# Performance work log

Measured on AMD Instinct MI355X. Metric: run time of the kernel, lower is better.

The kernel has to match this reference:

```python
import jax, jax.numpy as jnp
import numpy as np


def setup_inputs() -> dict:
    key = jax.random.key(0)
    k1, k2, k3, k4 = jax.random.split(key, 4)
    B, C, H, W = 32, 1, 512, 512
    return {
        "cancer_logits": jax.random.normal(k1, (B, C, H, W), dtype=jnp.float32),
        "label": jax.random.uniform(k2, (B,), dtype=jnp.float32),
        "prostate_mask": jax.random.uniform(k3, (B, 1, H, W), dtype=jnp.float32),
        "needle_mask": jax.random.uniform(k4, (B, 1, H, W), dtype=jnp.float32),
    }


def reference(cancer_logits, label, prostate_mask, needle_mask):
    # Valid region = prostate AND needle masks thresholded at 0.5.
    mask = (prostate_mask > 0.5) & (needle_mask > 0.5)          # [B,1,H,W] bool
    x = cancer_logits                                            # [B,1,H,W]
    y = label[:, None, None, None]                               # broadcast per-core label to pixels
    # Numerically-stable BCE with logits: max(x,0) - x*y + log(1+exp(-|x|))
    bce = jnp.maximum(x, 0.0) - x * y + jnp.log1p(jnp.exp(-jnp.abs(x)))
    m = mask.astype(x.dtype)
    # Mean over the selected (valid) elements == sum(bce*m)/count, same as
    # F.binary_cross_entropy_with_logits on the gathered logits/labels.
    count = jnp.maximum(jnp.sum(m), 1.0)
    return jnp.sum(bce * m) / count
```

## Files before the change

kernel.cpp:

```cpp
#include <hip/hip_runtime.h>
#include <math.h>

constexpr int HW_SIZE = 512 * 512;
constexpr int NB      = 32;
constexpr int N       = NB * HW_SIZE;
constexpr int N4      = N / 4;
constexpr int BLOCK   = 256;
constexpr int GRID1   = N4 / BLOCK;

__global__ __launch_bounds__(BLOCK) void loss_partial(
    const float4* __restrict__ x4,
    const float*  __restrict__ label,
    const float4* __restrict__ pm4,
    const float4* __restrict__ nm4,
    float2* __restrict__ partials) {
  const int i = blockIdx.x * BLOCK + threadIdx.x;
  const float y = label[blockIdx.x >> 8];

  const float4 xv = x4[i];
  const float4 pv = pm4[i];
  const float4 nv = nm4[i];

  float s_bce = 0.0f;
  float s_cnt = 0.0f;
  const float xs[4] = {xv.x, xv.y, xv.z, xv.w};
  const float ps[4] = {pv.x, pv.y, pv.z, pv.w};
  const float ns[4] = {nv.x, nv.y, nv.z, nv.w};
#pragma unroll
  for (int j = 0; j < 4; ++j) {
    const float m  = (fminf(ps[j], ns[j]) > 0.5f) ? 1.0f : 0.0f;
    const float xi = xs[j];
    const float sp  = __logf(1.0f + __expf(-fabsf(xi)));
    const float bce = fmaxf(xi, 0.0f) - xi * y + sp;
    s_bce = fmaf(bce, m, s_bce);
    s_cnt += m;
  }

#pragma unroll
  for (int off = 32; off > 0; off >>= 1) {
    s_bce += __shfl_down(s_bce, off);
    s_cnt += __shfl_down(s_cnt, off);
  }

  __shared__ float sb[4];
  __shared__ float sc[4];
  const int lane = threadIdx.x & 63;
  const int wave = threadIdx.x >> 6;
  if (lane == 0) {
    sb[wave] = s_bce;
    sc[wave] = s_cnt;
  }
  __syncthreads();
  if (threadIdx.x == 0) {
    partials[blockIdx.x] =
        make_float2(sb[0] + sb[1] + sb[2] + sb[3], sc[0] + sc[1] + sc[2] + sc[3]);
  }
}

__global__ __launch_bounds__(BLOCK) void loss_finalize(
    const float2* __restrict__ partials, float* __restrict__ out) {
  float s_bce = 0.0f;
  float s_cnt = 0.0f;
  const float4* p4 = (const float4*)partials;
  for (int i = threadIdx.x; i < GRID1 / 2; i += BLOCK) {
    const float4 v = p4[i];
    s_bce += v.x + v.z;
    s_cnt += v.y + v.w;
  }
#pragma unroll
  for (int off = 32; off > 0; off >>= 1) {
    s_bce += __shfl_down(s_bce, off);
    s_cnt += __shfl_down(s_cnt, off);
  }
  __shared__ float sb[4];
  __shared__ float sc[4];
  const int lane = threadIdx.x & 63;
  const int wave = threadIdx.x >> 6;
  if (lane == 0) {
    sb[wave] = s_bce;
    sc[wave] = s_cnt;
  }
  __syncthreads();
  if (threadIdx.x == 0) {
    const float tb = sb[0] + sb[1] + sb[2] + sb[3];
    const float tc = sc[0] + sc[1] + sc[2] + sc[3];
    out[0] = tb / fmaxf(tc, 1.0f);
  }
}

extern "C" void kernel_launch(void* const* d_in, const int* in_sizes, int n_in,
                              void* d_out, int out_size, void* d_ws, size_t ws_size,
                              hipStream_t stream) {
  const float4* x4    = (const float4*)d_in[0];
  const float*  label = (const float*)d_in[1];
  const float4* pm4   = (const float4*)d_in[2];
  const float4* nm4   = (const float4*)d_in[3];
  float2* partials = (float2*)d_ws;
  float*  out      = (float*)d_out;

  loss_partial<<<GRID1, BLOCK, 0, stream>>>(x4, label, pm4, nm4, partials);
  loss_finalize<<<1, BLOCK, 0, stream>>>(partials, out);
}
```

Before: 119.9 us.

## Process two float4 per thread, write per-wave partials, widen finalize

Each thread now loads two float4 from each input, halving the grid and increasing memory-level parallelism. A scheduling barrier keeps all loads issued before compute. The block-level shared-memory reduction is replaced by per-wave partial writes, and the finalize kernel uses 1024 threads with a fixed unrolled loop. This needs twice the partials workspace and adds some register pressure.

```diff
diff --git a/kernel.cpp b/kernel.cpp
--- a/kernel.cpp
+++ b/kernel.cpp
@@ -6,7 +6,9 @@
 constexpr int N       = NB * HW_SIZE;
 constexpr int N4      = N / 4;
 constexpr int BLOCK   = 256;
-constexpr int GRID1   = N4 / BLOCK;
+constexpr int K       = 2;
+constexpr int GRID1   = N4 / (BLOCK * K);
+constexpr int NWAVES  = GRID1 * (BLOCK / 64);
 
 __global__ __launch_bounds__(BLOCK) void loss_partial(
     const float4* __restrict__ x4,
@@ -14,20 +16,24 @@
     const float4* __restrict__ pm4,
     const float4* __restrict__ nm4,
     float2* __restrict__ partials) {
-  const int i = blockIdx.x * BLOCK + threadIdx.x;
-  const float y = label[blockIdx.x >> 8];
+  const int i = blockIdx.x * (BLOCK * K) + threadIdx.x;
+  const float y = label[blockIdx.x >> 7];
 
-  const float4 xv = x4[i];
-  const float4 pv = pm4[i];
-  const float4 nv = nm4[i];
+  const float4 xv0 = x4[i];
+  const float4 xv1 = x4[i + BLOCK];
+  const float4 pv0 = pm4[i];
+  const float4 pv1 = pm4[i + BLOCK];
+  const float4 nv0 = nm4[i];
+  const float4 nv1 = nm4[i + BLOCK];
+  __builtin_amdgcn_sched_barrier(0);
 
   float s_bce = 0.0f;
   float s_cnt = 0.0f;
-  const float xs[4] = {xv.x, xv.y, xv.z, xv.w};
-  const float ps[4] = {pv.x, pv.y, pv.z, pv.w};
-  const float ns[4] = {nv.x, nv.y, nv.z, nv.w};
+  const float xs[8] = {xv0.x, xv0.y, xv0.z, xv0.w, xv1.x, xv1.y, xv1.z, xv1.w};
+  const float ps[8] = {pv0.x, pv0.y, pv0.z, pv0.w, pv1.x, pv1.y, pv1.z, pv1.w};
+  const float ns[8] = {nv0.x, nv0.y, nv0.z, nv0.w, nv1.x, nv1.y, nv1.z, nv1.w};
 #pragma unroll
-  for (int j = 0; j < 4; ++j) {
+  for (int j = 0; j < 8; ++j) {
     const float m  = (fminf(ps[j], ns[j]) > 0.5f) ? 1.0f : 0.0f;
     const float xi = xs[j];
     const float sp  = __logf(1.0f + __expf(-fabsf(xi)));
@@ -41,9 +47,31 @@
     s_bce += __shfl_down(s_bce, off);
     s_cnt += __shfl_down(s_cnt, off);
   }
+  const int lane = threadIdx.x & 63;
+  const int wave = threadIdx.x >> 6;
+  if (lane == 0) {
+    partials[blockIdx.x * (BLOCK / 64) + wave] = make_float2(s_bce, s_cnt);
+  }
+}
 
-  __shared__ float sb[4];
-  __shared__ float sc[4];
+__global__ __launch_bounds__(1024) void loss_finalize(
+    const float2* __restrict__ partials, float* __restrict__ out) {
+  float s_bce = 0.0f;
+  float s_cnt = 0.0f;
+  const float4* p4 = (const float4*)partials;
+#pragma unroll
+  for (int k = 0; k < NWAVES / 2 / 1024; ++k) {
+    const float4 v = p4[k * 1024 + threadIdx.x];
+    s_bce += v.x + v.z;
+    s_cnt += v.y + v.w;
+  }
+#pragma unroll
+  for (int off = 32; off > 0; off >>= 1) {
+    s_bce += __shfl_down(s_bce, off);
+    s_cnt += __shfl_down(s_cnt, off);
+  }
+  __shared__ float sb[16];
+  __shared__ float sc[16];
   const int lane = threadIdx.x & 63;
   const int wave = threadIdx.x >> 6;
   if (lane == 0) {
@@ -52,38 +80,9 @@
   }
   __syncthreads();
   if (threadIdx.x == 0) {
-    partials[blockIdx.x] =
-        make_float2(sb[0] + sb[1] + sb[2] + sb[3], sc[0] + sc[1] + sc[2] + sc[3]);
-  }
-}
-
-__global__ __launch_bounds__(BLOCK) void loss_finalize(
-    const float2* __restrict__ partials, float* __restrict__ out) {
-  float s_bce = 0.0f;
-  float s_cnt = 0.0f;
-  const float4* p4 = (const float4*)partials;
-  for (int i = threadIdx.x; i < GRID1 / 2; i += BLOCK) {
-    const float4 v = p4[i];
-    s_bce += v.x + v.z;
-    s_cnt += v.y + v.w;
-  }
+    float tb = 0.0f, tc = 0.0f;
 #pragma unroll
-  for (int off = 32; off > 0; off >>= 1) {
-    s_bce += __shfl_down(s_bce, off);
-    s_cnt += __shfl_down(s_cnt, off);
-  }
-  __shared__ float sb[4];
-  __shared__ float sc[4];
-  const int lane = threadIdx.x & 63;
-  const int wave = threadIdx.x >> 6;
-  if (lane == 0) {
-    sb[wave] = s_bce;
-    sc[wave] = s_cnt;
-  }
-  __syncthreads();
-  if (threadIdx.x == 0) {
-    const float tb = sb[0] + sb[1] + sb[2] + sb[3];
-    const float tc = sc[0] + sc[1] + sc[2] + sc[3];
+    for (int w = 0; w < 16; ++w) { tb += sb[w]; tc += sc[w]; }
     out[0] = tb / fmaxf(tc, 1.0f);
   }
 }
@@ -99,5 +98,5 @@
   float*  out      = (float*)d_out;
 
   loss_partial<<<GRID1, BLOCK, 0, stream>>>(x4, label, pm4, nm4, partials);
-  loss_finalize<<<1, BLOCK, 0, stream>>>(partials, out);
+  loss_finalize<<<1, 1024, 0, stream>>>(partials, out);
 }
```

Result: no change. 118.6 us (-1.1%).
